# Optimization experiments

Measured on AMD Instinct MI355X. Metric: run time of the kernel, lower is better.

The kernel has to match this reference:

```python
import jax, jax.numpy as jnp
import numpy as np

N_NODES = 100000
N_EDGES = 1600000
T = 64          # num_timesteps (graphs)
D_IN = 256
D_H = 256
D_OUT = 16


def setup_inputs() -> dict:
    key = jax.random.key(0)
    ks = jax.random.split(key, 10)
    s = 1.0 / np.sqrt(D_H)
    x = jax.random.normal(ks[0], (N_NODES, D_IN), dtype=jnp.float32)
    edge_index = jax.random.randint(ks[1], (2, N_EDGES), 0, N_NODES, dtype=jnp.int64)
    ptr = (jnp.arange(T + 1, dtype=jnp.int64) * (N_NODES // T))  # even split of nodes into T snapshots
    return {
        "x": x,
        "edge_index": edge_index,
        "ptr": ptr,
        "W1": jax.random.normal(ks[2], (D_IN, D_H), dtype=jnp.float32) * s,
        "b1": jnp.zeros((D_H,), dtype=jnp.float32),
        "W2": jax.random.normal(ks[3], (D_H, D_H), dtype=jnp.float32) * s,
        "b2": jnp.zeros((D_H,), dtype=jnp.float32),
        "w_ih": jax.random.normal(ks[4], (3 * D_H, D_H), dtype=jnp.float32) * s,
        "w_hh": jax.random.normal(ks[5], (3 * D_H, D_H), dtype=jnp.float32) * s,
        "b_ih": jnp.zeros((3 * D_H,), dtype=jnp.float32),
        "b_hh": jnp.zeros((3 * D_H,), dtype=jnp.float32),
        "Wc": jax.random.normal(ks[6], (D_OUT, D_H), dtype=jnp.float32) * s,
        "bc": jnp.zeros((D_OUT,), dtype=jnp.float32),
    }


def _gcn_conv(x, W, b, src, dst, deg_inv_sqrt):
    # PyG GCNConv with self-loops: out_i = sum_j 1/sqrt(d_i d_j) * (x_j W) + (1/d_i) x_i W + b
    xw = x @ W                                            # [N, H]
    coef = deg_inv_sqrt[src] * deg_inv_sqrt[dst]          # [E]
    msg = xw[src] * coef[:, None]                         # [E, H] gather-scale
    agg = jax.ops.segment_sum(msg, dst, num_segments=N_NODES)
    return agg + xw * (deg_inv_sqrt ** 2)[:, None] + b


def _gru_final(seq, w_ih, w_hh, b_ih, b_hh):
    # torch nn.GRU, 1 layer, gate order (r, z, n). seq: [T, H] (batch=1)
    def step(h, x):
        gx = x @ w_ih.T + b_ih
        gh = h @ w_hh.T + b_hh
        xr, xz, xn = jnp.split(gx, 3)
        hr, hz, hn = jnp.split(gh, 3)
        r = jax.nn.sigmoid(xr + hr)
        z = jax.nn.sigmoid(xz + hz)
        n = jnp.tanh(xn + r * hn)
        h_new = (1.0 - z) * n + z * h
        return h_new, None
    h0 = jnp.zeros((D_H,), dtype=seq.dtype)
    h_final, _ = jax.lax.scan(step, h0, seq)
    return h_final


def reference(x, edge_index, ptr, W1, b1, W2, b2, w_ih, w_hh, b_ih, b_hh, Wc, bc):
    src, dst = edge_index[0], edge_index[1]
    # degree with self-loops
    deg = jax.ops.segment_sum(jnp.ones_like(dst, dtype=x.dtype), dst, num_segments=N_NODES) + 1.0
    deg_inv_sqrt = jax.lax.rsqrt(deg)

    h = jax.nn.relu(_gcn_conv(x, W1, b1, src, dst, deg_inv_sqrt))
    h = jax.nn.relu(_gcn_conv(h, W2, b2, src, dst, deg_inv_sqrt))

    # global_mean_pool over timestep segments derived from ptr
    seg = jnp.searchsorted(ptr, jnp.arange(N_NODES), side="right") - 1      # [N]
    sums = jax.ops.segment_sum(h, seg, num_segments=T)                       # [T, H]
    counts = (ptr[1:] - ptr[:-1]).astype(h.dtype)                            # [T]
    h_pooled = sums / jnp.maximum(counts, 1.0)[:, None]

    h_final = _gru_final(h_pooled, w_ih, w_hh, b_ih, b_hh)                   # [H]
    out = h_final @ Wc.T + bc                                                # [D_OUT]
    return out[None, :]                                                     # [1, D_OUT]
```

## Files before the change

kernel.cpp:

```cpp
#include <hip/hip_runtime.h>
#include <hip/hip_bf16.h>
#include <math.h>


static inline size_t align512(size_t x){ return (x + 511) & ~size_t(511); }

typedef _Float16 h2_t __attribute__((ext_vector_type(2)));
typedef unsigned short ushort_t;
typedef short bf16x8 __attribute__((ext_vector_type(8)));
typedef float f32x4 __attribute__((ext_vector_type(4)));
typedef float f32x2 __attribute__((ext_vector_type(2)));

#if defined(__has_builtin)
#if __has_builtin(__builtin_amdgcn_fdot2)
#define HAS_FDOT2 1
#endif
#if __has_builtin(__builtin_amdgcn_cvt_pk_f32_fp8) && __has_builtin(__builtin_amdgcn_cvt_pk_fp8_f32)
#define HAS_FP8CVT 1
#endif
#endif

__device__ inline ushort_t f2bf(float f){
  unsigned u = __float_as_uint(f);
  unsigned r = u + 0x7FFFu + ((u >> 16) & 1u);
  return (ushort_t)(r >> 16);
}
__device__ inline float bf2f(ushort_t h){ return __uint_as_float(((unsigned)h) << 16); }
__device__ inline unsigned pk2bf(float lo, float hi){
  return ((unsigned)f2bf(hi) << 16) | (unsigned)f2bf(lo);
}
__device__ inline bf16x8 as_bf16x8(uint4 u){
  union { uint4 u4; bf16x8 b; } c; c.u4 = u; return c.b;
}


__device__ inline unsigned char f2fp8(float x){
#ifdef HAS_FP8CVT
  int p = __builtin_amdgcn_cvt_pk_fp8_f32(x, x, 0, false);
  return (unsigned char)(p & 0xFF);
#else
  unsigned u = __float_as_uint(x);
  unsigned s = (u >> 24) & 0x80u;
  unsigned um = u & 0x7FFFFFFFu;
  if (um >= 0x43E00000u) return (unsigned char)(s | 0x7E);
  if (um <  0x3C000000u) return (unsigned char)s;
  unsigned r = um + 0x7FFFFu + ((um >> 20) & 1u);
  unsigned e = (r >> 23) & 0xFF, m = (r >> 20) & 7u;
  return (unsigned char)(s | ((e - 120u) << 3) | m);
#endif
}
__device__ inline void fp8x4_to_f32(unsigned v, float& a, float& b, float& c, float& d){
#ifdef HAS_FP8CVT
  f32x2 lo = __builtin_amdgcn_cvt_pk_f32_fp8(v, false);
  f32x2 hi = __builtin_amdgcn_cvt_pk_f32_fp8(v, true);
  a = lo.x; b = lo.y; c = hi.x; d = hi.y;
#else
  auto d1 = [](unsigned char t)->float{
    unsigned s = (t >> 7) & 1u, e = (t >> 3) & 0xFu, m = t & 7u;
    float v = (e == 0) ? ldexpf((float)m, -9) : ldexpf(8.0f + (float)m, (int)e - 10);
    return s ? -v : v;
  };
  a = d1(v & 0xFF); b = d1((v >> 8) & 0xFF); c = d1((v >> 16) & 0xFF); d = d1(v >> 24);
#endif
}


__global__ void count_kernel(const int* __restrict__ ei, int* __restrict__ cnt, int E){
  int e = blockIdx.x*256 + threadIdx.x;
  if (e < E) atomicAdd(&cnt[ei[E + e]], 1);
}

__global__ void dis_kernel(const int* __restrict__ cnt, float* __restrict__ dis, int N){
  int i = blockIdx.x*256 + threadIdx.x;
  if (i < N) dis[i] = rsqrtf((float)cnt[i] + 1.0f);
}

__global__ void scan_block_kernel(const int* __restrict__ cnt, int* __restrict__ rp,
                                  int* __restrict__ bsum, int N){
  __shared__ int s[2][1024];
  int t = threadIdx.x; int i = blockIdx.x*1024 + t;
  int v = (i < N) ? cnt[i] : 0;
  int cur = 0; s[0][t] = v; __syncthreads();
  for (int off = 1; off < 1024; off <<= 1){
    int nxt = cur ^ 1;
    int val = s[cur][t];
    if (t >= off) val += s[cur][t - off];
    s[nxt][t] = val; cur = nxt; __syncthreads();
  }
  if (i < N) rp[i+1] = s[cur][t];
  if (t == 1023) bsum[blockIdx.x] = s[cur][1023];
}

__global__ void scan_sums_kernel(int* __restrict__ bsum, int nb){
  __shared__ int s[128];
  int t = threadIdx.x;
  if (t < nb) s[t] = bsum[t];
  __syncthreads();
  if (t == 0){ int acc = 0; for (int b = 0; b < nb; b++){ int v = s[b]; s[b] = acc; acc += v; } }
  __syncthreads();
  if (t < nb) bsum[t] = s[t];
}

__global__ void add_off_kernel(int* __restrict__ rp, const int* __restrict__ bsum,
                               int* __restrict__ cnt, int N){
  int i = blockIdx.x*256 + threadIdx.x;
  if (i < N){ rp[i+1] += bsum[i >> 10]; cnt[i] = 0; }
  if (i == 0) rp[0] = 0;
}

__global__ void fill_kernel(const int* __restrict__ ei, const int* __restrict__ rp,
                            int* __restrict__ cnt, int* __restrict__ csrc, int E){
  int e = blockIdx.x*256 + threadIdx.x;
  if (e < E){
    int s = ei[e]; int d = ei[E + e];
    int pos = rp[d] + atomicAdd(&cnt[d], 1);
    csrc[pos] = s;
  }
}


__global__ void packW_kernel(const float* __restrict__ W, uint4* __restrict__ Wp){
  int idx = blockIdx.x*256 + threadIdx.x;
  int lane = idx & 63;
  int blk  = idx >> 6;
  int q    = blk & 7;
  int t16  = blk >> 3;
  int n = t16*16 + (lane & 15);
  int k = q*32 + (lane >> 4)*8;
  uint4 v;
  v.x = pk2bf(W[(size_t)(k+0)*256 + n], W[(size_t)(k+1)*256 + n]);
  v.y = pk2bf(W[(size_t)(k+2)*256 + n], W[(size_t)(k+3)*256 + n]);
  v.z = pk2bf(W[(size_t)(k+4)*256 + n], W[(size_t)(k+5)*256 + n]);
  v.w = pk2bf(W[(size_t)(k+6)*256 + n], W[(size_t)(k+7)*256 + n]);
  Wp[idx] = v;
}


template<bool A_BF16>
__global__ __launch_bounds__(256, 2) void gemm_mfma(const void* __restrict__ Ap,
                                                    const uint4* __restrict__ Wp,
                                                    unsigned char* __restrict__ out, int N){
  __shared__ __align__(16) ushort_t As[2][128][40];
  int tid  = threadIdx.x;
  int lane = tid & 63;
  int wave = tid >> 6;
  int wr = wave >> 1, wc = wave & 1;
  int quad = lane >> 4;
  int l15  = lane & 15;
  int r0 = blockIdx.x * 128;
  int cb = blockIdx.y;

  uint4 bfr[4][8];
  {
    const uint4* wpb = Wp + (size_t)(cb*2 + wc) * 2048;
    #pragma unroll
    for (int ct = 0; ct < 4; ct++)
      #pragma unroll
      for (int q = 0; q < 8; q++)
        bfr[ct][q] = wpb[(ct*8 + q)*64 + lane];
  }

  f32x4 acc[4][4];
  #pragma unroll
  for (int rt = 0; rt < 4; rt++)
    #pragma unroll
    for (int ct = 0; ct < 4; ct++)
      acc[rt][ct] = f32x4{0.f, 0.f, 0.f, 0.f};

  int srow = tid >> 1;
  int shalf = tid & 1;
  int grow = min(r0 + srow, N - 1);

  auto load_stage = [&](int it, uint4& v0, uint4& v1){
    int k0 = it*32 + shalf*16;
    if constexpr (A_BF16){
      const ushort_t* Ab = (const ushort_t*)Ap;
      const uint4* ga = (const uint4*)(Ab + (size_t)grow*256 + k0);
      v0 = ga[0]; v1 = ga[1];
    } else {
      const float* Af = (const float*)Ap;
      const float4* ga = (const float4*)(Af + (size_t)grow*256 + k0);
      float4 f0 = ga[0], f1 = ga[1], f2 = ga[2], f3 = ga[3];
      v0.x = pk2bf(f0.x, f0.y); v0.y = pk2bf(f0.z, f0.w);
      v0.z = pk2bf(f1.x, f1.y); v0.w = pk2bf(f1.z, f1.w);
      v1.x = pk2bf(f2.x, f2.y); v1.y = pk2bf(f2.z, f2.w);
      v1.z = pk2bf(f3.x, f3.y); v1.w = pk2bf(f3.z, f3.w);
    }
  };
  auto write_stage = [&](int b, uint4 v0, uint4 v1){
    *(uint4*)&As[b][srow][shalf*16]     = v0;
    *(uint4*)&As[b][srow][shalf*16 + 8] = v1;
  };

  {
    uint4 v0, v1;
    load_stage(0, v0, v1);
    write_stage(0, v0, v1);
  }
  __syncthreads();

  #pragma unroll
  for (int it = 0; it < 8; it++){
    const int b = it & 1;
    uint4 n0, n1;
    if (it < 7) load_stage(it + 1, n0, n1);
    #pragma unroll
    for (int rt = 0; rt < 4; rt++){
      int arow = wr*64 + rt*16 + l15;
      uint4 av = *(const uint4*)&As[b][arow][quad*8];
      bf16x8 af = as_bf16x8(av);
      #pragma unroll
      for (int ct = 0; ct < 4; ct++)
        acc[rt][ct] = __builtin_amdgcn_mfma_f32_16x16x32_bf16(
            af, as_bf16x8(bfr[ct][it]), acc[rt][ct], 0, 0, 0);
    }
    if (it < 7){
      write_stage(b ^ 1, n0, n1);
      __syncthreads();
    }
  }

  int crow0 = r0 + wr*64 + quad*4;
  int ccol0 = cb*128 + wc*64 + l15;
  #pragma unroll
  for (int rt = 0; rt < 4; rt++){
    #pragma unroll
    for (int g = 0; g < 4; g++){
      int row = crow0 + rt*16 + g;
      if (row < N){
        #pragma unroll
        for (int ct = 0; ct < 4; ct++)
          out[(size_t)row*256 + ccol0 + ct*16] = f2fp8(acc[rt][ct][g]);
      }
    }
  }
}


__global__ __launch_bounds__(256) void agg_kernel(const unsigned char* __restrict__ xw,
                                                  const float* __restrict__ dis,
                                                  const int* __restrict__ rp,
                                                  const int* __restrict__ csrc,
                                                  const float* __restrict__ bias,
                                                  ushort_t* __restrict__ out, int N){
  int node = blockIdx.x*8 + (threadIdx.x >> 5);
  int lane = threadIdx.x & 31;
  if (node >= N) return;
  const uint2* xw2 = (const uint2*)xw;
  float di = dis[node];
  float sc = di * di;
  float acc[8];
  {
    uint2 a = xw2[(size_t)node*32 + lane];
    float v0,v1,v2,v3,v4,v5,v6,v7;
    fp8x4_to_f32(a.x, v0, v1, v2, v3);
    fp8x4_to_f32(a.y, v4, v5, v6, v7);
    acc[0]=v0*sc; acc[1]=v1*sc; acc[2]=v2*sc; acc[3]=v3*sc;
    acc[4]=v4*sc; acc[5]=v5*sc; acc[6]=v6*sc; acc[7]=v7*sc;
  }
  int e0 = rp[node], e1 = rp[node+1];
  for (int e = e0; e < e1; e++){
    int s = csrc[e];
    float cc = dis[s] * di;
    uint2 v = xw2[(size_t)s*32 + lane];
    float v0,v1,v2,v3,v4,v5,v6,v7;
    fp8x4_to_f32(v.x, v0, v1, v2, v3);
    fp8x4_to_f32(v.y, v4, v5, v6, v7);
    acc[0] = fmaf(v0, cc, acc[0]);
    acc[1] = fmaf(v1, cc, acc[1]);
    acc[2] = fmaf(v2, cc, acc[2]);
    acc[3] = fmaf(v3, cc, acc[3]);
    acc[4] = fmaf(v4, cc, acc[4]);
    acc[5] = fmaf(v5, cc, acc[5]);
    acc[6] = fmaf(v6, cc, acc[6]);
    acc[7] = fmaf(v7, cc, acc[7]);
  }
  const float4* b4 = (const float4*)bias;
  float4 bA = b4[lane*2], bB = b4[lane*2+1];
  acc[0] = fmaxf(acc[0] + bA.x, 0.f);
  acc[1] = fmaxf(acc[1] + bA.y, 0.f);
  acc[2] = fmaxf(acc[2] + bA.z, 0.f);
  acc[3] = fmaxf(acc[3] + bA.w, 0.f);
  acc[4] = fmaxf(acc[4] + bB.x, 0.f);
  acc[5] = fmaxf(acc[5] + bB.y, 0.f);
  acc[6] = fmaxf(acc[6] + bB.z, 0.f);
  acc[7] = fmaxf(acc[7] + bB.w, 0.f);
  uint4 o;
  o.x = pk2bf(acc[0], acc[1]);
  o.y = pk2bf(acc[2], acc[3]);
  o.z = pk2bf(acc[4], acc[5]);
  o.w = pk2bf(acc[6], acc[7]);
  ((uint4*)out)[(size_t)node*32 + lane] = o;
}


__global__ void pool_kernel(const ushort_t* __restrict__ h, const int* __restrict__ ptr,
                            float* __restrict__ hp){
  int t = blockIdx.x; int part = blockIdx.y; int c = threadIdx.x;
  int s0 = ptr[t], s1 = ptr[t+1];
  int len = s1 - s0;
  int chunk = (len + 7) / 8;
  int r0 = s0 + part*chunk;
  int r1 = min(r0 + chunk, s1);
  float acc = 0.f;
  for (int r = r0; r < r1; r++) acc += bf2f(h[(size_t)r*256 + c]);
  if (r1 > r0) atomicAdd(&hp[t*256 + c], acc);
}


__global__ __launch_bounds__(768) void gx_kernel(const float* __restrict__ hp,
                                                 const int* __restrict__ ptr,
                                                 const float* __restrict__ wih,
                                                 const float* __restrict__ bih,
                                                 const float* __restrict__ bhh,
                                                 float* __restrict__ gx){
  __shared__ float xs[256];
  int t = blockIdx.x; int g = threadIdx.x;
  if (g < 256){
    float cf = (float)max(ptr[t+1] - ptr[t], 1);
    xs[g] = hp[t*256 + g] / cf;
  }
  __syncthreads();
  float acc = bih[g] + (g < 512 ? bhh[g] : 0.f);
  const float* wr = wih + (size_t)g*256;
  #pragma unroll 4
  for (int k = 0; k < 256; k++) acc = fmaf(xs[k], wr[k], acc);
  gx[t*768 + g] = acc;
}


__device__ inline float fast_sig(float x){
  return __builtin_amdgcn_rcpf(1.f + __expf(-x));
}
__device__ inline float fast_tanh(float x){
  return 1.f - 2.f*__builtin_amdgcn_rcpf(1.f + __expf(2.f*x));
}

__global__ __launch_bounds__(512, 1) void gru_kernel(const float* __restrict__ gx,
                                                     const float* __restrict__ whh,
                                                     const float* __restrict__ bhh,
                                                     const float* __restrict__ Wc,
                                                     const float* __restrict__ bc,
                                                     float* __restrict__ out){
  __shared__ __align__(16) _Float16 hh[2][256];
  __shared__ float hfin[256];
  int tid = threadIdx.x;
  int i = tid >> 1;
  int half = tid & 1;

  h2_t wr[64], wz[64], wn[64];
  {
    const float2* w2 = (const float2*)whh;
    size_t base = (size_t)half * 64;
    const float2* pr = w2 + (size_t)i*128       + base;
    const float2* pz = w2 + (size_t)(i+256)*128 + base;
    const float2* pn = w2 + (size_t)(i+512)*128 + base;
    #pragma unroll
    for (int k = 0; k < 64; k++){
      float2 a = pr[k];
      float2 b = pz[k];
      float2 c = pn[k];
      wr[k] = h2_t{(_Float16)a.x, (_Float16)a.y};
      wz[k] = h2_t{(_Float16)b.x, (_Float16)b.y};
      wn[k] = h2_t{(_Float16)c.x, (_Float16)c.y};
    }
  }
  float bN = bhh[i + 512];
  if (tid < 256) hh[0][tid] = (_Float16)0.f;
  float h = 0.f;
  float gxr = gx[i], gxz = gx[256 + i], gxn = gx[512 + i];
  __syncthreads();

  for (int t = 0; t < 64; t++){
    float ngr = 0.f, ngz = 0.f, ngn = 0.f;
    if (t < 63){
      const float* g = gx + (size_t)(t+1)*768;
      ngr = g[i]; ngz = g[256 + i]; ngn = g[512 + i];
    }
    const h2_t* hp2 = ((const h2_t*)hh[t & 1]) + half*64;
    float aR0=0.f, aR1=0.f, aZ0=0.f, aZ1=0.f, aN0=0.f, aN1=0.f;
    #pragma unroll
    for (int k = 0; k < 64; k += 2){
      h2_t h0 = hp2[k];
      h2_t h1 = hp2[k+1];
#ifdef HAS_FDOT2
      aR0 = __builtin_amdgcn_fdot2(h0, wr[k],   aR0, false);
      aZ0 = __builtin_amdgcn_fdot2(h0, wz[k],   aZ0, false);
      aN0 = __builtin_amdgcn_fdot2(h0, wn[k],   aN0, false);
      aR1 = __builtin_amdgcn_fdot2(h1, wr[k+1], aR1, false);
      aZ1 = __builtin_amdgcn_fdot2(h1, wz[k+1], aZ1, false);
      aN1 = __builtin_amdgcn_fdot2(h1, wn[k+1], aN1, false);
#else
      aR0 = fmaf((float)h0.x, (float)wr[k].x, aR0);
      aR0 = fmaf((float)h0.y, (float)wr[k].y, aR0);
      aZ0 = fmaf((float)h0.x, (float)wz[k].x, aZ0);
      aZ0 = fmaf((float)h0.y, (float)wz[k].y, aZ0);
      aN0 = fmaf((float)h0.x, (float)wn[k].x, aN0);
      aN0 = fmaf((float)h0.y, (float)wn[k].y, aN0);
      aR1 = fmaf((float)h1.x, (float)wr[k+1].x, aR1);
      aR1 = fmaf((float)h1.y, (float)wr[k+1].y, aR1);
      aZ1 = fmaf((float)h1.x, (float)wz[k+1].x, aZ1);
      aZ1 = fmaf((float)h1.y, (float)wz[k+1].y, aZ1);
      aN1 = fmaf((float)h1.x, (float)wn[k+1].x, aN1);
      aN1 = fmaf((float)h1.y, (float)wn[k+1].y, aN1);
#endif
    }
    float accR = aR0 + aR1, accZ = aZ0 + aZ1, accN = aN0 + aN1;
    accR += __shfl_xor(accR, 1);
    accZ += __shfl_xor(accZ, 1);
    accN += __shfl_xor(accN, 1);
    float r = fast_sig(gxr + accR);
    float z = fast_sig(gxz + accZ);
    float n = fast_tanh(gxn + r*(accN + bN));
    float hnew = (1.f - z)*n + z*h;
    if (half == 0) hh[(t & 1) ^ 1][i] = (_Float16)hnew;
    gxr = ngr; gxz = ngz; gxn = ngn;
    h = hnew;
    __syncthreads();
  }

  if (half == 0) hfin[i] = h;
  __syncthreads();
  if (tid < 64){
    int r = tid >> 2, qq = tid & 3;
    const float4* wrow = (const float4*)(Wc + (size_t)r*256 + (size_t)qq*64);
    const float4* hv = (const float4*)(hfin + (size_t)qq*64);
    float acc = 0.f;
    #pragma unroll
    for (int k = 0; k < 16; k++){
      float4 wv = wrow[k];
      float4 xv = hv[k];
      acc = fmaf(wv.x, xv.x, acc);
      acc = fmaf(wv.y, xv.y, acc);
      acc = fmaf(wv.z, xv.z, acc);
      acc = fmaf(wv.w, xv.w, acc);
    }
    acc += __shfl_xor(acc, 1);
    acc += __shfl_xor(acc, 2);
    if (qq == 0) out[r] = acc + bc[r];
  }
}

extern "C" void kernel_launch(void* const* d_in, const int* in_sizes, int n_in,
                              void* d_out, int out_size, void* d_ws, size_t ws_size,
                              hipStream_t stream){
  const float* x   = (const float*)d_in[0];
  const int*   ei  = (const int*)d_in[1];
  const int*   ptr = (const int*)d_in[2];
  const float* W1  = (const float*)d_in[3];
  const float* b1  = (const float*)d_in[4];
  const float* W2  = (const float*)d_in[5];
  const float* b2  = (const float*)d_in[6];
  const float* wih = (const float*)d_in[7];
  const float* whh = (const float*)d_in[8];
  const float* bih = (const float*)d_in[9];
  const float* bhh = (const float*)d_in[10];
  const float* Wc  = (const float*)d_in[11];
  const float* bc  = (const float*)d_in[12];
  float* outp = (float*)d_out;

  const int N = in_sizes[0] / 256;
  const int E = in_sizes[1] / 2;

  char* w = (char*)d_ws;
  size_t off = 0;
  auto alloc = [&](size_t bytes){ void* p = w + off; off = align512(off + bytes); return p; };
  unsigned char* bufA = (unsigned char*)alloc((size_t)N*256);
  ushort_t*      bufB = (ushort_t*)alloc((size_t)N*256*2);
  float* dis  = (float*)alloc((size_t)N*4);
  int*   cnt  = (int*)  alloc((size_t)N*4);
  int*   rp   = (int*)  alloc((size_t)(N+1)*4);
  int*   bsum = (int*)  alloc(128*4);
  int*   csrc = (int*)  alloc((size_t)E*4);
  uint4* Wp1  = (uint4*)alloc(8192*16);
  uint4* Wp2  = (uint4*)alloc(8192*16);
  float* hp   = (float*)alloc((size_t)64*256*4);
  float* gxb  = (float*)alloc((size_t)64*768*4);
  (void)ws_size; (void)n_in; (void)out_size;

  hipMemsetAsync(cnt, 0, (size_t)N*4, stream);
  hipMemsetAsync(hp,  0, (size_t)64*256*4, stream);

  count_kernel<<<(E+255)/256, 256, 0, stream>>>(ei, cnt, E);
  dis_kernel<<<(N+255)/256, 256, 0, stream>>>(cnt, dis, N);
  int nb = (N + 1023) / 1024;
  scan_block_kernel<<<nb, 1024, 0, stream>>>(cnt, rp, bsum, N);
  scan_sums_kernel<<<1, 128, 0, stream>>>(bsum, nb);
  add_off_kernel<<<(N+255)/256, 256, 0, stream>>>(rp, bsum, cnt, N);
  fill_kernel<<<(E+255)/256, 256, 0, stream>>>(ei, rp, cnt, csrc, E);
  packW_kernel<<<32, 256, 0, stream>>>(W1, Wp1);
  packW_kernel<<<32, 256, 0, stream>>>(W2, Wp2);

  gemm_mfma<false><<<dim3((N+127)/128, 2), 256, 0, stream>>>(x, Wp1, bufA, N);
  agg_kernel<<<(N+7)/8, 256, 0, stream>>>(bufA, dis, rp, csrc, b1, bufB, N);
  gemm_mfma<true><<<dim3((N+127)/128, 2), 256, 0, stream>>>(bufB, Wp2, bufA, N);
  agg_kernel<<<(N+7)/8, 256, 0, stream>>>(bufA, dis, rp, csrc, b2, bufB, N);

  pool_kernel<<<dim3(64, 8), 256, 0, stream>>>(bufB, ptr, hp);
  gx_kernel<<<64, 768, 0, stream>>>(hp, ptr, wih, bih, bhh, gxb);
  gru_kernel<<<1, 512, 0, stream>>>(gxb, whh, bhh, Wc, bc, outp);
}
```

Before: 833.4 us.

## Split GRU recurrent weights across registers, LDS and streamed global loads

A new pack kernel converts w_hh to fp16 and lays it out per thread, split into three parts. One part stays in registers, one sits in LDS, and the remainder is reloaded each timestep from two duplicated global copies. This replaces the 192 per-thread h2 weight registers, which likely spilled or limited scheduling. The change adds an extra launch, per-step global loads, and heavy LDS use, and it drops the prefetch of the next gx.

```diff
diff --git a/kernel.cpp b/kernel.cpp
--- a/kernel.cpp
+++ b/kernel.cpp
@@ -31,6 +31,16 @@
 }
 __device__ inline bf16x8 as_bf16x8(uint4 u){
   union { uint4 u4; bf16x8 b; } c; c.u4 = u; return c.b;
+}
+__device__ inline h2_t u2h2(unsigned u){
+  union { unsigned u; h2_t h; } c; c.u = u; return c.h;
+}
+__device__ inline float fdot2a(h2_t a, h2_t b, float c){
+#ifdef HAS_FDOT2
+  return __builtin_amdgcn_fdot2(a, b, c, false);
+#else
+  return fmaf((float)a.x, (float)b.x, fmaf((float)a.y, (float)b.y, c));
+#endif
 }
 
 
@@ -133,6 +143,46 @@
   v.z = pk2bf(W[(size_t)(k+4)*256 + n], W[(size_t)(k+5)*256 + n]);
   v.w = pk2bf(W[(size_t)(k+6)*256 + n], W[(size_t)(k+7)*256 + n]);
   Wp[idx] = v;
+}
+
+#define WHHP_LBASE 45056u
+#define WHHP_SBASE 81920u
+#define WHHP_SREP  16384u
+#define WHHP_TOTAL 114688u
+
+__global__ void packWhh_kernel(const float* __restrict__ whh, unsigned* __restrict__ wp){
+  int idx = blockIdx.x*256 + threadIdx.x;
+  if (idx >= 98304) return;
+  int t = idx / 192;
+  int m = idx - t*192;
+  int i = t >> 1, half = t & 1;
+  int g  = m >> 6;
+  int mg = m & 63;
+  int c = mg >> 3, j = mg & 7;
+  int hk = half*64 + c*8 + j;
+  int row = i + g*256;
+  float a = whh[(size_t)row*256 + 2*hk];
+  float b = whh[(size_t)row*256 + 2*hk + 1];
+  union { _Float16 f[2]; unsigned u; } cv;
+  cv.f[0] = (_Float16)a; cv.f[1] = (_Float16)b;
+  if (g == 0){
+    int s = c*8 + j;
+    wp[(unsigned)((s >> 2)*2048 + t*4 + (s & 3))] = cv.u;
+  } else if (g == 1 && c < 3){
+    int s = 64 + c*8 + j;
+    wp[(unsigned)((s >> 2)*2048 + t*4 + (s & 3))] = cv.u;
+  } else if (g == 1){
+    int li = (c-3)*8 + j;
+    wp[WHHP_LBASE + (unsigned)((li >> 1)*1024 + t*2 + (li & 1))] = cv.u;
+  } else if (c < 4){
+    int li = 40 + c*8 + j;
+    wp[WHHP_LBASE + (unsigned)((li >> 1)*1024 + t*2 + (li & 1))] = cv.u;
+  } else {
+    int si = (c-4)*8 + j;
+    unsigned so = (unsigned)((si >> 2)*2048 + t*4 + (si & 3));
+    wp[WHHP_SBASE + so] = cv.u;
+    wp[WHHP_SBASE + WHHP_SREP + so] = cv.u;
+  }
 }
 
 
@@ -337,73 +387,90 @@
 }
 
 __global__ __launch_bounds__(512, 1) void gru_kernel(const float* __restrict__ gx,
-                                                     const float* __restrict__ whh,
+                                                     const unsigned* __restrict__ whhp,
                                                      const float* __restrict__ bhh,
                                                      const float* __restrict__ Wc,
                                                      const float* __restrict__ bc,
                                                      float* __restrict__ out){
+  __shared__ uint2 lw2[36*512];
   __shared__ __align__(16) _Float16 hh[2][256];
   __shared__ float hfin[256];
   int tid = threadIdx.x;
   int i = tid >> 1;
   int half = tid & 1;
 
-  h2_t wr[64], wz[64], wn[64];
+  uint4 wreg4[22];
   {
-    const float2* w2 = (const float2*)whh;
-    size_t base = (size_t)half * 64;
-    const float2* pr = w2 + (size_t)i*128       + base;
-    const float2* pz = w2 + (size_t)(i+256)*128 + base;
-    const float2* pn = w2 + (size_t)(i+512)*128 + base;
-    #pragma unroll
-    for (int k = 0; k < 64; k++){
-      float2 a = pr[k];
-      float2 b = pz[k];
-      float2 c = pn[k];
-      wr[k] = h2_t{(_Float16)a.x, (_Float16)a.y};
-      wz[k] = h2_t{(_Float16)b.x, (_Float16)b.y};
-      wn[k] = h2_t{(_Float16)c.x, (_Float16)c.y};
-    }
-  }
+    const uint4* R4 = (const uint4*)whhp;
+    #pragma unroll
+    for (int j = 0; j < 22; j++) wreg4[j] = R4[j*512 + tid];
+  }
+  {
+    const uint2* Lz2 = (const uint2*)(whhp + WHHP_LBASE);
+    #pragma unroll
+    for (int r = 0; r < 36; r++) lw2[r*512 + tid] = Lz2[r*512 + tid];
+  }
+
   float bN = bhh[i + 512];
   if (tid < 256) hh[0][tid] = (_Float16)0.f;
   float h = 0.f;
-  float gxr = gx[i], gxz = gx[256 + i], gxn = gx[512 + i];
   __syncthreads();
 
+  #pragma unroll 1
   for (int t = 0; t < 64; t++){
-    float ngr = 0.f, ngz = 0.f, ngn = 0.f;
-    if (t < 63){
-      const float* g = gx + (size_t)(t+1)*768;
-      ngr = g[i]; ngz = g[256 + i]; ngn = g[512 + i];
-    }
-    const h2_t* hp2 = ((const h2_t*)hh[t & 1]) + half*64;
+    const float* gxt = gx + (size_t)t*768;
+    float gxr = gxt[i], gxz = gxt[256 + i], gxn = gxt[512 + i];
+    const uint4* hh4 = (const uint4*)((const char*)hh + ((t & 1) << 9) + (half << 8));
+    const uint4* S4 = (const uint4*)(whhp + WHHP_SBASE + ((unsigned)(t & 1))*WHHP_SREP);
+    uint4 s0 = S4[0*512 + tid], s1 = S4[1*512 + tid];
+    uint4 s2, s3, s4, s5, s6, s7;
     float aR0=0.f, aR1=0.f, aZ0=0.f, aZ1=0.f, aN0=0.f, aN1=0.f;
     #pragma unroll
-    for (int k = 0; k < 64; k += 2){
-      h2_t h0 = hp2[k];
-      h2_t h1 = hp2[k+1];
-#ifdef HAS_FDOT2
-      aR0 = __builtin_amdgcn_fdot2(h0, wr[k],   aR0, false);
-      aZ0 = __builtin_amdgcn_fdot2(h0, wz[k],   aZ0, false);
-      aN0 = __builtin_amdgcn_fdot2(h0, wn[k],   aN0, false);
-      aR1 = __builtin_amdgcn_fdot2(h1, wr[k+1], aR1, false);
-      aZ1 = __builtin_amdgcn_fdot2(h1, wz[k+1], aZ1, false);
-      aN1 = __builtin_amdgcn_fdot2(h1, wn[k+1], aN1, false);
-#else
-      aR0 = fmaf((float)h0.x, (float)wr[k].x, aR0);
-      aR0 = fmaf((float)h0.y, (float)wr[k].y, aR0);
-      aZ0 = fmaf((float)h0.x, (float)wz[k].x, aZ0);
-      aZ0 = fmaf((float)h0.y, (float)wz[k].y, aZ0);
-      aN0 = fmaf((float)h0.x, (float)wn[k].x, aN0);
-      aN0 = fmaf((float)h0.y, (float)wn[k].y, aN0);
-      aR1 = fmaf((float)h1.x, (float)wr[k+1].x, aR1);
-      aR1 = fmaf((float)h1.y, (float)wr[k+1].y, aR1);
-      aZ1 = fmaf((float)h1.x, (float)wz[k+1].x, aZ1);
-      aZ1 = fmaf((float)h1.y, (float)wz[k+1].y, aZ1);
-      aN1 = fmaf((float)h1.x, (float)wn[k+1].x, aN1);
-      aN1 = fmaf((float)h1.y, (float)wn[k+1].y, aN1);
-#endif
+    for (int c = 0; c < 8; c++){
+      if (c == 2){ s2 = S4[2*512 + tid]; s3 = S4[3*512 + tid]; }
+      if (c == 4){ s4 = S4[4*512 + tid]; s5 = S4[5*512 + tid]; }
+      if (c == 5){ s6 = S4[6*512 + tid]; s7 = S4[7*512 + tid]; }
+      uint4 hA = hh4[c*2], hB = hh4[c*2 + 1];
+      h2_t h0=u2h2(hA.x), h1=u2h2(hA.y), h2v=u2h2(hA.z), h3=u2h2(hA.w);
+      h2_t h4=u2h2(hB.x), h5=u2h2(hB.y), h6v=u2h2(hB.z), h7=u2h2(hB.w);
+      {
+        uint4 wa = wreg4[c*2], wb = wreg4[c*2 + 1];
+        aR0 = fdot2a(h0,  u2h2(wa.x), aR0); aR1 = fdot2a(h1, u2h2(wa.y), aR1);
+        aR0 = fdot2a(h2v, u2h2(wa.z), aR0); aR1 = fdot2a(h3, u2h2(wa.w), aR1);
+        aR0 = fdot2a(h4,  u2h2(wb.x), aR0); aR1 = fdot2a(h5, u2h2(wb.y), aR1);
+        aR0 = fdot2a(h6v, u2h2(wb.z), aR0); aR1 = fdot2a(h7, u2h2(wb.w), aR1);
+      }
+      if (c < 3){
+        uint4 za = wreg4[16 + c*2], zb = wreg4[17 + c*2];
+        aZ0 = fdot2a(h0,  u2h2(za.x), aZ0); aZ1 = fdot2a(h1, u2h2(za.y), aZ1);
+        aZ0 = fdot2a(h2v, u2h2(za.z), aZ0); aZ1 = fdot2a(h3, u2h2(za.w), aZ1);
+        aZ0 = fdot2a(h4,  u2h2(zb.x), aZ0); aZ1 = fdot2a(h5, u2h2(zb.y), aZ1);
+        aZ0 = fdot2a(h6v, u2h2(zb.z), aZ0); aZ1 = fdot2a(h7, u2h2(zb.w), aZ1);
+      } else {
+        int pb = (c - 3)*4;
+        uint2 z0 = lw2[(pb+0)*512 + tid], z1 = lw2[(pb+1)*512 + tid];
+        uint2 z2 = lw2[(pb+2)*512 + tid], z3 = lw2[(pb+3)*512 + tid];
+        aZ0 = fdot2a(h0,  u2h2(z0.x), aZ0); aZ1 = fdot2a(h1, u2h2(z0.y), aZ1);
+        aZ0 = fdot2a(h2v, u2h2(z1.x), aZ0); aZ1 = fdot2a(h3, u2h2(z1.y), aZ1);
+        aZ0 = fdot2a(h4,  u2h2(z2.x), aZ0); aZ1 = fdot2a(h5, u2h2(z2.y), aZ1);
+        aZ0 = fdot2a(h6v, u2h2(z3.x), aZ0); aZ1 = fdot2a(h7, u2h2(z3.y), aZ1);
+      }
+      if (c < 4){
+        int pb = 20 + c*4;
+        uint2 n0 = lw2[(pb+0)*512 + tid], n1 = lw2[(pb+1)*512 + tid];
+        uint2 n2 = lw2[(pb+2)*512 + tid], n3 = lw2[(pb+3)*512 + tid];
+        aN0 = fdot2a(h0,  u2h2(n0.x), aN0); aN1 = fdot2a(h1, u2h2(n0.y), aN1);
+        aN0 = fdot2a(h2v, u2h2(n1.x), aN0); aN1 = fdot2a(h3, u2h2(n1.y), aN1);
+        aN0 = fdot2a(h4,  u2h2(n2.x), aN0); aN1 = fdot2a(h5, u2h2(n2.y), aN1);
+        aN0 = fdot2a(h6v, u2h2(n3.x), aN0); aN1 = fdot2a(h7, u2h2(n3.y), aN1);
+      } else {
+        uint4 na = (c == 4) ? s0 : (c == 5) ? s2 : (c == 6) ? s4 : s6;
+        uint4 nb = (c == 4) ? s1 : (c == 5) ? s3 : (c == 6) ? s5 : s7;
+        aN0 = fdot2a(h0,  u2h2(na.x), aN0); aN1 = fdot2a(h1, u2h2(na.y), aN1);
+        aN0 = fdot2a(h2v, u2h2(na.z), aN0); aN1 = fdot2a(h3, u2h2(na.w), aN1);
+        aN0 = fdot2a(h4,  u2h2(nb.x), aN0); aN1 = fdot2a(h5, u2h2(nb.y), aN1);
+        aN0 = fdot2a(h6v, u2h2(nb.z), aN0); aN1 = fdot2a(h7, u2h2(nb.w), aN1);
+      }
     }
     float accR = aR0 + aR1, accZ = aZ0 + aZ1, accN = aN0 + aN1;
     accR += __shfl_xor(accR, 1);
@@ -414,7 +481,6 @@
     float n = fast_tanh(gxn + r*(accN + bN));
     float hnew = (1.f - z)*n + z*h;
     if (half == 0) hh[(t & 1) ^ 1][i] = (_Float16)hnew;
-    gxr = ngr; gxz = ngz; gxn = ngn;
     h = hnew;
     __syncthreads();
   }
@@ -474,6 +540,7 @@
   int*   csrc = (int*)  alloc((size_t)E*4);
   uint4* Wp1  = (uint4*)alloc(8192*16);
   uint4* Wp2  = (uint4*)alloc(8192*16);
+  unsigned* whhp = (unsigned*)alloc((size_t)WHHP_TOTAL*4);
   float* hp   = (float*)alloc((size_t)64*256*4);
   float* gxb  = (float*)alloc((size_t)64*768*4);
   (void)ws_size; (void)n_in; (void)out_size;
@@ -490,6 +557,7 @@
   fill_kernel<<<(E+255)/256, 256, 0, stream>>>(ei, rp, cnt, csrc, E);
   packW_kernel<<<32, 256, 0, stream>>>(W1, Wp1);
   packW_kernel<<<32, 256, 0, stream>>>(W2, Wp2);
+  packWhh_kernel<<<384, 256, 0, stream>>>(whh, whhp);
 
   gemm_mfma<false><<<dim3((N+127)/128, 2), 256, 0, stream>>>(x, Wp1, bufA, N);
   agg_kernel<<<(N+7)/8, 256, 0, stream>>>(bufA, dis, rp, csrc, b1, bufB, N);
@@ -498,5 +566,5 @@
 
   pool_kernel<<<dim3(64, 8), 256, 0, stream>>>(bufB, ptr, hp);
   gx_kernel<<<64, 768, 0, stream>>>(hp, ptr, wih, bih, bhh, gxb);
-  gru_kernel<<<1, 512, 0, stream>>>(gxb, whh, bhh, Wc, bc, outp);
-}
+  gru_kernel<<<1, 512, 0, stream>>>(gxb, whhp, bhh, Wc, bc, outp);
+}
```

Result: faster. 784.9 us (-5.8%).
